# Optimization experiments

Measured on AMD Instinct MI355X. Metric: run time of the kernel, lower is better.

Reference implementation:

```python
import jax, jax.numpy as jnp
import numpy as np

WIN_H, WIN_W = 7, 7
NUM_HEADS = 16
DIM = 512
HEAD_DIM = DIM // NUM_HEADS
SCALE = HEAD_DIM ** -0.5


def rel_pos_index(h, w):
    # Faithful port of get_relative_position_index
    xx, yy = jnp.meshgrid(jnp.arange(h), jnp.arange(w), indexing='ij')
    coords = jnp.stack([yy, xx], axis=0).reshape(2, -1)  # (2, N)
    rel = coords[:, :, None] - coords[:, None, :]        # (2, N, N)
    return (rel[0] + h - 1) * (2 * w - 1) + (rel[1] + w - 1)  # (N, N)


def setup_inputs() -> dict:
    key = jax.random.key(0)
    ks = jax.random.split(key, 5)
    B_, N, C = 4096, WIN_H * WIN_W, DIM
    num_win = 64
    return {
        'x': jax.random.normal(ks[0], (B_, N, C), dtype=jnp.float32),
        'mask': jnp.zeros((num_win, N, N), dtype=jnp.float32),  # 0/-inf shift mask; zeros = no shift
        'qkv_w': jax.random.normal(ks[1], (C, 3 * C), dtype=jnp.float32) * 0.02,
        'qkv_b': jnp.zeros((3 * C,), dtype=jnp.float32),
        'proj_w': jax.random.normal(ks[2], (C, C), dtype=jnp.float32) * 0.02,
        'proj_b': jnp.zeros((C,), dtype=jnp.float32),
        'bias_table': jax.random.normal(ks[3], ((2 * WIN_H - 1) * (2 * WIN_W - 1), NUM_HEADS), dtype=jnp.float32) * 0.02,
    }


def reference(x, mask, qkv_w, qkv_b, proj_w, proj_b, bias_table):
    B_, N, C = x.shape
    H, hd = NUM_HEADS, HEAD_DIM
    qkv = x @ qkv_w + qkv_b                                  # (B_, N, 3C)
    qkv = qkv.reshape(B_, N, 3, H, hd).transpose(2, 0, 3, 1, 4)  # (3, B_, H, N, hd)
    q, k, v = qkv[0], qkv[1], qkv[2]
    q = q * jnp.asarray(SCALE, dtype=qkv.dtype)
    attn = jnp.einsum('bhnd,bhmd->bhnm', q, k)               # (B_, H, N, N)
    idx = rel_pos_index(WIN_H, WIN_W)                        # (N, N)
    bias = bias_table[idx].transpose(2, 0, 1)                # (H, N, N)
    attn = attn + bias
    num_win = mask.shape[0]
    attn = attn.reshape(B_ // num_win, num_win, H, N, N) + mask[None, :, None]
    attn = jax.nn.softmax(attn.reshape(B_, H, N, N), axis=-1)
    out = jnp.einsum('bhnm,bhmd->bhnd', attn, v)             # (B_, H, N, hd)
    out = out.transpose(0, 2, 1, 3).reshape(B_, N, C)
    return out @ proj_w + proj_b
```

## Files before the change

kernel.cpp:

```cpp
#include <hip/hip_runtime.h>
#include <stdint.h>

#define WIN_N 49
#define NH 16
#define HD 32
#define CDIM 512
#define NB 4096
#define M_ROWS (NB * WIN_N)
#define QKV_N 1536
#define SCALE_Q 0.17677669529663689f

typedef __attribute__((ext_vector_type(8))) short bf16x8;
typedef __attribute__((ext_vector_type(4))) float f32x4;

__device__ __forceinline__ unsigned short f2bf(float f) {
  unsigned int u = __float_as_uint(f);
  u += 0x7fff + ((u >> 16) & 1);
  return (unsigned short)(u >> 16);
}
__device__ __forceinline__ unsigned int pack2(float a, float b) {
  return (unsigned int)f2bf(a) | ((unsigned int)f2bf(b) << 16);
}

typedef const __attribute__((address_space(1))) unsigned int* gas1_t;
typedef __attribute__((address_space(3))) unsigned int* las3_t;
#define GL2LDS(g, l) __builtin_amdgcn_global_load_lds((gas1_t)(g), (las3_t)(l), 16, 0, 0)

__global__ void prep_weights(const float* __restrict__ qkv_w,
                             const float* __restrict__ proj_w,
                             unsigned short* __restrict__ wqkv_t,
                             unsigned short* __restrict__ wproj_t) {
  int i = blockIdx.x * blockDim.x + threadIdx.x;
  if (i < QKV_N * CDIM) {
    int n = i >> 9, k = i & 511;
    wqkv_t[i] = f2bf(qkv_w[k * QKV_N + n]);
  } else {
    int j = i - QKV_N * CDIM;
    if (j < CDIM * CDIM) {
      int n = j >> 9, k = j & 511;
      wproj_t[j] = f2bf(proj_w[k * CDIM + n]);
    }
  }
}

__global__ void conv_x(const float* __restrict__ x,
                       unsigned short* __restrict__ xb, int n8) {
  int i = blockIdx.x * blockDim.x + threadIdx.x;
  const int stride = gridDim.x * blockDim.x;
  for (; i < n8; i += stride) {
    const float4* p = (const float4*)(x + (size_t)i * 8);
    float4 a = p[0], b = p[1];
    *(uint4*)(xb + (size_t)i * 8) =
        make_uint4(pack2(a.x, a.y), pack2(a.z, a.w), pack2(b.x, b.y), pack2(b.z, b.w));
  }
}

template <bool OUT_F32>
__global__ __launch_bounds__(256) void gemm_bt(
    const unsigned short* __restrict__ A, int lda,
    const unsigned short* __restrict__ Bt,
    void* __restrict__ Cptr, int ldc,
    const float* __restrict__ bias,
    int K, int scale_cols, float scale) {
  __shared__ __align__(16) unsigned short As[128 * 32];
  __shared__ __align__(16) unsigned short Bs[128 * 32];
  const int tid = threadIdx.x;
  const int bm = blockIdx.y * 128;
  const int bn = blockIdx.x * 128;
  const int lane = tid & 63, wid = tid >> 6;
  const int wm = (wid & 1) * 64, wn = (wid >> 1) * 64;
  const int quad = lane >> 4, l16 = lane & 15;
  const int r0 = tid >> 2;
  const int c0 = (tid & 3) * 8;

  unsigned short* AsW = As + wid * 512;
  unsigned short* BsW = Bs + wid * 512;

  const f32x4 fzero = {0.f, 0.f, 0.f, 0.f};
  f32x4 acc[4][4];
#pragma unroll
  for (int i = 0; i < 4; i++)
#pragma unroll
    for (int j = 0; j < 4; j++) acc[i][j] = fzero;

  const unsigned short* pA = A + (size_t)(bm + r0) * lda + c0;
  const unsigned short* pB = Bt + (size_t)(bn + r0) * K + c0;
  const size_t a64 = (size_t)64 * lda;
  const size_t b64 = (size_t)64 * K;

  for (int kk = 0; kk < K; kk += 32) {
    GL2LDS(pA + kk, AsW);
    GL2LDS(pA + kk + a64, AsW + 2048);
    GL2LDS(pB + kk, BsW);
    GL2LDS(pB + kk + b64, BsW + 2048);
    __syncthreads();
    bf16x8 a[4], b[4];
#pragma unroll
    for (int i = 0; i < 4; i++) a[i] = *(const bf16x8*)&As[(wm + i * 16 + l16) * 32 + quad * 8];
#pragma unroll
    for (int i = 0; i < 4; i++) b[i] = *(const bf16x8*)&Bs[(wn + i * 16 + l16) * 32 + quad * 8];
#pragma unroll
    for (int i = 0; i < 4; i++)
#pragma unroll
      for (int j = 0; j < 4; j++)
        acc[i][j] = __builtin_amdgcn_mfma_f32_16x16x32_bf16(a[i], b[j], acc[i][j], 0, 0, 0);
    __syncthreads();
  }

#pragma unroll
  for (int i = 0; i < 4; i++) {
    const int row = bm + wm + i * 16 + quad * 4;
#pragma unroll
    for (int j = 0; j < 4; j++) {
      const int col = bn + wn + j * 16 + l16;
      const float bv = bias[col];
      const float sc = (col < scale_cols) ? scale : 1.0f;
#pragma unroll
      for (int r = 0; r < 4; r++) {
        float v = (acc[i][j][r] + bv) * sc;
        if constexpr (OUT_F32)
          ((float*)Cptr)[(size_t)(row + r) * ldc + col] = v;
        else
          ((unsigned short*)Cptr)[(size_t)(row + r) * ldc + col] = f2bf(v);
      }
    }
  }
}

__global__ __launch_bounds__(256) void attn_mfma(
    unsigned short* __restrict__ qkv,
    const float* __restrict__ bias_table,
    const float* __restrict__ mask) {
  const int PS = 72;
  const int VS = 64;
  __shared__ __align__(16) unsigned short Pl_all[4][64 * 72];
  __shared__ __align__(16) unsigned short Vt_all[4][32 * 64];
  const int tid = threadIdx.x;
  const int wid = tid >> 6, lane = tid & 63;
  const int quad = lane >> 4, l16 = lane & 15;
  const int b = blockIdx.x;
  const int h = blockIdx.y * 4 + wid;
  unsigned short* Pl = Pl_all[wid];
  unsigned short* Vt = Vt_all[wid];
  const size_t row0 = (size_t)b * WIN_N;

  bf16x8 aq[4], bk[4];
#pragma unroll
  for (int i = 0; i < 4; i++) {
    size_t r = row0 + i * 16 + l16;
    if (r > (size_t)(M_ROWS - 1)) r = M_ROWS - 1;
    const unsigned short* pq = qkv + r * QKV_N + h * HD + quad * 8;
    aq[i] = *(const bf16x8*)pq;
    bk[i] = *(const bf16x8*)(pq + 512);
  }

  {
    const int m = lane;
    if (m < WIN_N) {
      const unsigned short* pv = qkv + (row0 + m) * QKV_N + 1024 + h * HD;
      uint4 tv[4];
      tv[0] = *(const uint4*)(pv + 0);
      tv[1] = *(const uint4*)(pv + 8);
      tv[2] = *(const uint4*)(pv + 16);
      tv[3] = *(const uint4*)(pv + 24);
      const unsigned short* tmp = (const unsigned short*)tv;
#pragma unroll
      for (int d = 0; d < 32; d++) Vt[d * VS + m] = tmp[d];
    } else {
#pragma unroll
      for (int d = 0; d < 32; d++) Vt[d * VS + m] = 0;
    }
  }

  const f32x4 fzero = {0.f, 0.f, 0.f, 0.f};
  f32x4 s[4][4];
#pragma unroll
  for (int i = 0; i < 4; i++)
#pragma unroll
    for (int j = 0; j < 4; j++)
      s[i][j] = __builtin_amdgcn_mfma_f32_16x16x32_bf16(aq[i], bk[j], fzero, 0, 0, 0);

  const float* mrow = mask + (size_t)(b & 63) * (WIN_N * WIN_N);
#pragma unroll
  for (int i = 0; i < 4; i++) {
#pragma unroll
    for (int r = 0; r < 4; r++) {
      const int t = i * 16 + quad * 4 + r;
      const int ti = t / 7, tj = t % 7;
      float v[4];
#pragma unroll
      for (int j = 0; j < 4; j++) {
        const int m = j * 16 + l16;
        float x = s[i][j][r];
        if (t < WIN_N && m < WIN_N) {
          const int mi = m / 7, mj = m % 7;
          const int idx = (tj - mj + 6) * 13 + (ti - mi + 6);
          x += bias_table[idx * NH + h] + mrow[t * WIN_N + m];
        }
        if (m >= WIN_N) x = -3.0e38f;
        v[j] = x;
      }
      float mx = fmaxf(fmaxf(v[0], v[1]), fmaxf(v[2], v[3]));
      mx = fmaxf(mx, __shfl_xor(mx, 1));
      mx = fmaxf(mx, __shfl_xor(mx, 2));
      mx = fmaxf(mx, __shfl_xor(mx, 4));
      mx = fmaxf(mx, __shfl_xor(mx, 8));
      float p[4];
      float sum = 0.f;
#pragma unroll
      for (int j = 0; j < 4; j++) {
        p[j] = __expf(v[j] - mx);
        sum += p[j];
      }
      sum += __shfl_xor(sum, 1);
      sum += __shfl_xor(sum, 2);
      sum += __shfl_xor(sum, 4);
      sum += __shfl_xor(sum, 8);
      const float inv = 1.0f / sum;
#pragma unroll
      for (int j = 0; j < 4; j++) Pl[t * PS + j * 16 + l16] = f2bf(p[j] * inv);
    }
  }
  __syncthreads();

  f32x4 o[4][2];
#pragma unroll
  for (int i = 0; i < 4; i++)
#pragma unroll
    for (int ni = 0; ni < 2; ni++) o[i][ni] = fzero;
#pragma unroll
  for (int ki = 0; ki < 2; ki++) {
    bf16x8 bv[2];
#pragma unroll
    for (int ni = 0; ni < 2; ni++)
      bv[ni] = *(const bf16x8*)&Vt[(ni * 16 + l16) * VS + ki * 32 + quad * 8];
#pragma unroll
    for (int i = 0; i < 4; i++) {
      bf16x8 ap = *(const bf16x8*)&Pl[(i * 16 + l16) * PS + ki * 32 + quad * 8];
#pragma unroll
      for (int ni = 0; ni < 2; ni++)
        o[i][ni] = __builtin_amdgcn_mfma_f32_16x16x32_bf16(ap, bv[ni], o[i][ni], 0, 0, 0);
    }
  }

#pragma unroll
  for (int i = 0; i < 4; i++) {
#pragma unroll
    for (int r = 0; r < 4; r++) {
      const int t = i * 16 + quad * 4 + r;
      if (t < WIN_N) {
        unsigned short* po = qkv + (row0 + t) * QKV_N + h * HD;
        po[l16] = f2bf(o[i][0][r]);
        po[16 + l16] = f2bf(o[i][1][r]);
      }
    }
  }
}

extern "C" void kernel_launch(void* const* d_in, const int* in_sizes, int n_in,
                              void* d_out, int out_size, void* d_ws, size_t ws_size,
                              hipStream_t stream) {
  const float* x = (const float*)d_in[0];
  const float* mask = (const float*)d_in[1];
  const float* qkv_w = (const float*)d_in[2];
  const float* qkv_b = (const float*)d_in[3];
  const float* proj_w = (const float*)d_in[4];
  const float* proj_b = (const float*)d_in[5];
  const float* bias_table = (const float*)d_in[6];
  float* out = (float*)d_out;

  unsigned short* qkvb = (unsigned short*)d_ws;
  unsigned short* wqkv_t = qkvb + (size_t)M_ROWS * QKV_N;
  unsigned short* wproj_t = wqkv_t + (size_t)QKV_N * CDIM;

  unsigned short* xb = (unsigned short*)d_out;

  prep_weights<<<4096, 256, 0, stream>>>(qkv_w, proj_w, wqkv_t, wproj_t);
  conv_x<<<2048, 256, 0, stream>>>(x, xb, (M_ROWS * CDIM) / 8);

  gemm_bt<false><<<dim3(QKV_N / 128, M_ROWS / 128), 256, 0, stream>>>(
      xb, CDIM, wqkv_t, qkvb, QKV_N, qkv_b, CDIM, 512, SCALE_Q);

  attn_mfma<<<dim3(NB, NH / 4), 256, 0, stream>>>(qkvb, bias_table, mask);

  gemm_bt<true><<<dim3(CDIM / 128, M_ROWS / 128), 256, 0, stream>>>(
      qkvb, QKV_N, wproj_t, out, CDIM, proj_b, CDIM, 0, 1.0f);
}
```

Measured before the change: 1.840 ms.

## Double-buffer GEMM LDS tiles, swizzle block order, stage bf16 output through LDS

The GEMM K-loop now uses two LDS buffers, so the next tile's global-to-LDS load is issued while the current tile runs MFMAs, and there is one barrier per step instead of two. Workgroup indices are remapped in an interleaved order to improve L2 reuse of the A and B tiles. The bf16 output path writes the tile into LDS first and then stores it with coalesced 16-byte writes instead of scattered 2-byte stores. Costs are double the LDS footprint, which may lower occupancy, and the loop assumes K is a multiple of 64 and the block count is divisible by 8.

```diff
diff --git a/kernel.cpp b/kernel.cpp
--- a/kernel.cpp
+++ b/kernel.cpp
@@ -62,20 +62,22 @@
     void* __restrict__ Cptr, int ldc,
     const float* __restrict__ bias,
     int K, int scale_cols, float scale) {
-  __shared__ __align__(16) unsigned short As[128 * 32];
-  __shared__ __align__(16) unsigned short Bs[128 * 32];
+  __shared__ __align__(16) unsigned short SB[4][128 * 32];
   const int tid = threadIdx.x;
-  const int bm = blockIdx.y * 128;
-  const int bn = blockIdx.x * 128;
+
+  const int gx = gridDim.x;
+  const int nwg = gx * gridDim.y;
+  int lin = blockIdx.y * gx + blockIdx.x;
+  lin = (lin & 7) * (nwg >> 3) + (lin >> 3);
+  const int bm = (lin / gx) * 128;
+  const int bn = (lin % gx) * 128;
+
   const int lane = tid & 63, wid = tid >> 6;
   const int wm = (wid & 1) * 64, wn = (wid >> 1) * 64;
   const int quad = lane >> 4, l16 = lane & 15;
   const int r0 = tid >> 2;
   const int c0 = (tid & 3) * 8;
 
-  unsigned short* AsW = As + wid * 512;
-  unsigned short* BsW = Bs + wid * 512;
-
   const f32x4 fzero = {0.f, 0.f, 0.f, 0.f};
   f32x4 acc[4][4];
 #pragma unroll
@@ -87,42 +89,80 @@
   const unsigned short* pB = Bt + (size_t)(bn + r0) * K + c0;
   const size_t a64 = (size_t)64 * lda;
   const size_t b64 = (size_t)64 * K;
-
-  for (int kk = 0; kk < K; kk += 32) {
-    GL2LDS(pA + kk, AsW);
-    GL2LDS(pA + kk + a64, AsW + 2048);
-    GL2LDS(pB + kk, BsW);
-    GL2LDS(pB + kk + b64, BsW + 2048);
+  const int woff = wid * 512;
+
+#define STAGE(ab, bb, kk_)                              \
+  do {                                                  \
+    GL2LDS(pA + (kk_), SB[ab] + woff);                  \
+    GL2LDS(pA + (kk_) + a64, SB[ab] + woff + 2048);     \
+    GL2LDS(pB + (kk_), SB[bb] + woff);                  \
+    GL2LDS(pB + (kk_) + b64, SB[bb] + woff + 2048);     \
+  } while (0)
+
+#define COMPUTE(ab, bb)                                                          \
+  do {                                                                           \
+    bf16x8 a[4], b[4];                                                           \
+    _Pragma("unroll") for (int i = 0; i < 4; i++)                                \
+        a[i] = *(const bf16x8*)&SB[ab][(wm + i * 16 + l16) * 32 + quad * 8];     \
+    _Pragma("unroll") for (int i = 0; i < 4; i++)                                \
+        b[i] = *(const bf16x8*)&SB[bb][(wn + i * 16 + l16) * 32 + quad * 8];     \
+    _Pragma("unroll") for (int i = 0; i < 4; i++)                                \
+        _Pragma("unroll") for (int j = 0; j < 4; j++)                            \
+            acc[i][j] = __builtin_amdgcn_mfma_f32_16x16x32_bf16(a[i], b[j],      \
+                                                                acc[i][j], 0, 0, 0); \
+  } while (0)
+
+  const int nt = K >> 5;
+  STAGE(0, 1, 0);
+  for (int t = 0; t < nt; t += 2) {
     __syncthreads();
-    bf16x8 a[4], b[4];
-#pragma unroll
-    for (int i = 0; i < 4; i++) a[i] = *(const bf16x8*)&As[(wm + i * 16 + l16) * 32 + quad * 8];
-#pragma unroll
-    for (int i = 0; i < 4; i++) b[i] = *(const bf16x8*)&Bs[(wn + i * 16 + l16) * 32 + quad * 8];
-#pragma unroll
-    for (int i = 0; i < 4; i++)
-#pragma unroll
-      for (int j = 0; j < 4; j++)
-        acc[i][j] = __builtin_amdgcn_mfma_f32_16x16x32_bf16(a[i], b[j], acc[i][j], 0, 0, 0);
+    STAGE(2, 3, (t + 1) * 32);
+    COMPUTE(0, 1);
     __syncthreads();
-  }
-
-#pragma unroll
-  for (int i = 0; i < 4; i++) {
-    const int row = bm + wm + i * 16 + quad * 4;
-#pragma unroll
-    for (int j = 0; j < 4; j++) {
-      const int col = bn + wn + j * 16 + l16;
-      const float bv = bias[col];
-      const float sc = (col < scale_cols) ? scale : 1.0f;
-#pragma unroll
-      for (int r = 0; r < 4; r++) {
-        float v = (acc[i][j][r] + bv) * sc;
-        if constexpr (OUT_F32)
-          ((float*)Cptr)[(size_t)(row + r) * ldc + col] = v;
-        else
-          ((unsigned short*)Cptr)[(size_t)(row + r) * ldc + col] = f2bf(v);
-      }
+    if (t + 2 < nt) STAGE(0, 1, (t + 2) * 32);
+    COMPUTE(2, 3);
+  }
+#undef STAGE
+#undef COMPUTE
+
+  if constexpr (OUT_F32) {
+#pragma unroll
+    for (int i = 0; i < 4; i++) {
+      const int row = bm + wm + i * 16 + quad * 4;
+#pragma unroll
+      for (int j = 0; j < 4; j++) {
+        const int col = bn + wn + j * 16 + l16;
+        const float bv = bias[col];
+#pragma unroll
+        for (int r = 0; r < 4; r++)
+          ((float*)Cptr)[(size_t)(row + r) * ldc + col] = acc[i][j][r] + bv;
+      }
+    }
+  } else {
+    unsigned short* Ct = &SB[0][0];
+    __syncthreads();
+#pragma unroll
+    for (int i = 0; i < 4; i++) {
+#pragma unroll
+      for (int j = 0; j < 4; j++) {
+        const int colg = bn + wn + j * 16 + l16;
+        const float bv = bias[colg];
+        const float sc = (colg < scale_cols) ? scale : 1.0f;
+        const int coll = wn + j * 16 + l16;
+#pragma unroll
+        for (int r = 0; r < 4; r++) {
+          const int rowl = wm + i * 16 + quad * 4 + r;
+          Ct[rowl * 128 + coll] = f2bf((acc[i][j][r] + bv) * sc);
+        }
+      }
+    }
+    __syncthreads();
+#pragma unroll
+    for (int tt = 0; tt < 8; tt++) {
+      const int row = tt * 16 + (tid >> 4);
+      const int ce = (tid & 15) * 8;
+      uint4 vv = *(const uint4*)&Ct[row * 128 + ce];
+      *(uint4*)&((unsigned short*)Cptr)[(size_t)(bm + row) * ldc + bn + ce] = vv;
     }
   }
 }
```

After: 1.831 ms. No clear change (-0.5%).
